# Optimization experiments

Measured on AMD Instinct MI355X. Metric: run time of the kernel, lower is better.

The kernel has to match this reference:

```python
import jax, jax.numpy as jnp
import numpy as np

NEMB = 128
N_NODES = 8192
N_EDGES = 16384
N_STEMS = 4096
N_GRAPHS = 256
N_BLOCKS = 105       # BlockDictionary.n_unique_blocks
N_STEMTYPES = 32     # BlockDictionary.n_stem_types
OUT_PER_STEM = 105
OUT_PER_STOP = 1
NUM_CONV_STEPS = 12
SLOPE = 0.01         # nn.LeakyReLU default negative slope


def _act(v):
    return jax.nn.leaky_relu(v, SLOPE)


def setup_inputs() -> dict:
    key = jax.random.key(0)
    ks = jax.random.split(key, 32)
    def p(i, shape, fan_in):
        return jax.random.normal(ks[i], shape, jnp.float32) / np.sqrt(fan_in).astype(np.float32)
    D = NEMB
    inp = {
        "x": jax.random.randint(ks[0], (N_NODES,), 0, N_BLOCKS + 1),
        "stemtypes": jax.random.randint(ks[1], (N_STEMS,), 0, N_STEMTYPES + 1),
        "edge_attr": jax.random.randint(ks[2], (N_EDGES, 2), 0, N_STEMTYPES),
        "edge_index": jax.random.randint(ks[3], (2, N_EDGES), 0, N_NODES),
        "stem_node_idx": jax.random.randint(ks[4], (N_STEMS,), 0, N_NODES),
        "node_batch": jnp.sort(jax.random.randint(ks[5], (N_NODES,), 0, N_GRAPHS)),
        # embedding tables
        "emb_block": p(6, (N_BLOCKS + 1, D), D),
        "emb_stem": p(7, (N_STEMTYPES + 1, D), D),
        "emb_bond": p(8, (N_STEMTYPES, D), D),
        # block2emb MLP
        "b2e_w1": p(9, (D, D), D), "b2e_b1": p(10, (D,), D),
        "b2e_w2": p(11, (D, D), D), "b2e_b2": p(12, (D,), D),
        # NNConv root weight + bias (edge-nn is identity: nn.Sequential())
        "conv_root": p(13, (D, D), D), "conv_bias": p(14, (D,), D),
        # GRU (torch gate order r, z, n)
        "gru_w_ih": p(15, (3 * D, D), D), "gru_w_hh": p(16, (3 * D, D), D),
        "gru_b_ih": p(17, (3 * D,), D), "gru_b_hh": p(18, (3 * D,), D),
        # stem2pred MLP (in = 2*D)
        "s2p_w1": p(19, (D, 2 * D), 2 * D), "s2p_b1": p(20, (D,), 2 * D),
        "s2p_w2": p(21, (D, D), D), "s2p_b2": p(22, (D,), D),
        "s2p_w3": p(23, (OUT_PER_STEM, D), D), "s2p_b3": p(24, (OUT_PER_STEM,), D),
        # global2pred MLP
        "g2p_w1": p(25, (D, D), D), "g2p_b1": p(26, (D,), D),
        "g2p_w2": p(27, (OUT_PER_STOP, D), D), "g2p_b2": p(28, (OUT_PER_STOP,), D),
    }
    return inp


def reference(x, stemtypes, edge_attr, edge_index, stem_node_idx, node_batch,
              emb_block, emb_stem, emb_bond,
              b2e_w1, b2e_b1, b2e_w2, b2e_b2,
              conv_root, conv_bias,
              gru_w_ih, gru_w_hh, gru_b_ih, gru_b_hh,
              s2p_w1, s2p_b1, s2p_w2, s2p_b2, s2p_w3, s2p_b3,
              g2p_w1, g2p_b1, g2p_w2, g2p_b2):
    block_emb = emb_block[x]                          # [N, D]
    stem_emb = emb_stem[stemtypes]                    # [S, D]
    be = emb_bond[edge_attr]                          # [E, 2, D]
    # outer product -> per-edge [D_in, D_out] weight (matches view(-1, in, out))
    W_e = be[:, 0, :, None] * be[:, 1, None, :]       # [E, D, D]

    out = _act(block_emb @ b2e_w1.T + b2e_b1) @ b2e_w2.T + b2e_b2  # [N, D]
    h = out                                           # GRU hidden state

    src, dst = edge_index[0], edge_index[1]
    ones_e = jnp.ones((N_EDGES,), out.dtype)
    deg = jax.ops.segment_sum(ones_e, dst, num_segments=N_NODES)
    inv_deg = jnp.where(deg > 0, 1.0 / jnp.maximum(deg, 1.0), 0.0)[:, None]

    for _ in range(NUM_CONV_STEPS):
        # NNConv: mean_j (x_j @ W_e) + x @ root + bias, then LeakyReLU
        msg = jnp.einsum('ei,eij->ej', out[src], W_e)                  # [E, D]
        agg = jax.ops.segment_sum(msg, dst, num_segments=N_NODES) * inv_deg
        m = _act(agg + out @ conv_root + conv_bias)
        # single-layer GRU, seq_len = 1
        gi = m @ gru_w_ih.T + gru_b_ih
        gh = h @ gru_w_hh.T + gru_b_hh
        ir, iz, inn = jnp.split(gi, 3, axis=-1)
        hr, hz, hn = jnp.split(gh, 3, axis=-1)
        r = jax.nn.sigmoid(ir + hr)
        z = jax.nn.sigmoid(iz + hz)
        n = jnp.tanh(inn + r * hn)
        h = (1.0 - z) * n + z * h
        out = h

    stem_cat = jnp.concatenate([out[stem_node_idx], stem_emb], axis=1)  # [S, 2D]
    s = _act(stem_cat @ s2p_w1.T + s2p_b1)
    s = _act(s @ s2p_w2.T + s2p_b2)
    stem_pred = s @ s2p_w3.T + s2p_b3                                   # [S, out_per_stem]

    # global_mean_pool
    gsum = jax.ops.segment_sum(out, node_batch, num_segments=N_GRAPHS)
    gcnt = jax.ops.segment_sum(jnp.ones((N_NODES,), out.dtype), node_batch, num_segments=N_GRAPHS)
    gmean = gsum / jnp.maximum(gcnt, 1.0)[:, None]
    g = _act(gmean @ g2p_w1.T + g2p_b1)
    stop_pred = g @ g2p_w2.T + g2p_b2                                   # [G, out_per_stop]
    return stem_pred, stop_pred
```

## Files before the change

kernel.cpp:

```cpp
#include <hip/hip_runtime.h>
#include <math.h>

#define D 128
#define NNODES 8192
#define NEDGES 16384
#define NSTEMS 4096
#define NGRAPHS 256
#define NSTEPS 12
#define OPS 105
#define SLOPE 0.01f
#define MT 32
#define NB (NNODES / MT)
#define ECAP 512
#define LDA 136
#define LDA2 264
#define LDQ 40
#define LDH 132

typedef _Float16 half_t;
typedef __attribute__((ext_vector_type(8))) _Float16 f16x8;
typedef __attribute__((ext_vector_type(4))) float f32x4;

__device__ __forceinline__ float leaky(float x) { return x > 0.f ? x : SLOPE * x; }
__device__ __forceinline__ float fast_sigmoid(float x) {
    return __builtin_amdgcn_rcpf(1.f + __expf(-x));
}
__device__ __forceinline__ float fast_tanh(float x) {
    float e = __expf(2.f * x);
    return 1.f - 2.f * __builtin_amdgcn_rcpf(e + 1.f);
}

__device__ __forceinline__ void gbar_arrive(int* bar, int sync_no) {
    __syncthreads();
    if (threadIdx.x == 0) {
        int grp = blockIdx.x >> 5;
        int old = __hip_atomic_fetch_add(&bar[grp * 32], 1,
                                         __ATOMIC_RELEASE, __HIP_MEMORY_SCOPE_AGENT);
        if (old == sync_no * 32 - 1) {
            int r = __hip_atomic_fetch_add(&bar[256], 1,
                                           __ATOMIC_RELEASE, __HIP_MEMORY_SCOPE_AGENT);
            if (r == sync_no * 8 - 1)
                __hip_atomic_store(&bar[288], sync_no,
                                   __ATOMIC_RELEASE, __HIP_MEMORY_SCOPE_AGENT);
        }
    }
}
__device__ __forceinline__ void gbar_wait(int* bar, int sync_no) {
    if (threadIdx.x == 0) {
        while (__hip_atomic_load(&bar[288], __ATOMIC_RELAXED,
                                 __HIP_MEMORY_SCOPE_AGENT) < sync_no)
            __builtin_amdgcn_s_sleep(1);
    }
    __syncthreads();
}

__global__ void k_setup(
    const float* __restrict__ root, const float* __restrict__ wih,
    const float* __restrict__ whh, const float* __restrict__ bond,
    const float* __restrict__ sw1, const float* __restrict__ sw2,
    const float* __restrict__ sw3, const float* __restrict__ bw1,
    const float* __restrict__ bw2, const float* __restrict__ gw1,
    half_t* __restrict__ rootP, half_t* __restrict__ WihP,
    half_t* __restrict__ WhhP, half_t* __restrict__ bondTP,
    half_t* __restrict__ s1P, half_t* __restrict__ s2P, half_t* __restrict__ s3P,
    half_t* __restrict__ w1P, half_t* __restrict__ w2P, half_t* __restrict__ bondQP,
    float* __restrict__ g1T, int* __restrict__ zeroi) {
    int idx = blockIdx.x * 256 + threadIdx.x;
    int which = blockIdx.y;
    if (which == 10) {
        if (idx < 128 * 128) {
            int r = idx >> 7, c = idx & 127;
            g1T[c * 128 + r] = gw1[idx];
        }
        return;
    }
    if (which == 11) {
        if (idx < 512) zeroi[idx] = 0;
        return;
    }
    int KT = (which == 4) ? 8 : (which == 9) ? 1 : 4;
    int NT = (which == 1 || which == 2) ? 24 : (which == 3) ? 2 : (which == 6) ? 7 : 8;
    if (idx >= NT * KT * 512) return;
    int j = idx & 7;
    int L = (idx >> 3) & 63;
    int t = idx >> 9;
    int kt = t % KT, nt = t / KT;
    int k = kt * 32 + (L >> 4) * 8 + j;
    int n = nt * 16 + (L & 15);
    switch (which) {
        case 0: rootP[idx] = (half_t)root[k * D + n]; break;
        case 1: WihP[idx] = (half_t)wih[n * D + k]; break;
        case 2: WhhP[idx] = (half_t)whh[n * D + k]; break;
        case 3: bondTP[idx] = (half_t)bond[n * D + k]; break;
        case 4: s1P[idx] = (half_t)sw1[n * 256 + k]; break;
        case 5: s2P[idx] = (half_t)sw2[n * 128 + k]; break;
        case 6: s3P[idx] = (n < OPS) ? (half_t)sw3[n * 128 + k] : (half_t)0.f; break;
        case 7: w1P[idx] = (half_t)bw1[n * D + k]; break;
        case 8: w2P[idx] = (half_t)bw2[n * D + k]; break;
        case 9: bondQP[idx] = (half_t)bond[k * D + n]; break;
    }
}

__device__ __forceinline__ int lower_bound_dev(const int* a, int n, int v) {
    int lo = 0, hi = n;
    while (lo < hi) {
        int m = (lo + hi) >> 1;
        if (a[m] < v) lo = m + 1;
        else hi = m;
    }
    return lo;
}

__global__ __launch_bounds__(512, 2) void k_fused(
    const int* __restrict__ x, const float* __restrict__ embBlock,
    const half_t* __restrict__ w1P, const float* __restrict__ b1i,
    const half_t* __restrict__ w2P, const float* __restrict__ b2i,
    const half_t* __restrict__ rootP, const half_t* __restrict__ WihP,
    const half_t* __restrict__ WhhP, const half_t* __restrict__ bondTP,
    const half_t* __restrict__ bondQP,
    const float* __restrict__ cbias, const float* __restrict__ bih,
    const float* __restrict__ bhh,
    const int* __restrict__ eidx, const int* __restrict__ eattr,
    float* __restrict__ Pbuf0, float* __restrict__ Pbuf1,
    float* __restrict__ hF,
    const int* __restrict__ sni, const int* __restrict__ stypes,
    const float* __restrict__ embStem,
    const half_t* __restrict__ s1P, const float* __restrict__ sb1,
    const half_t* __restrict__ s2P, const float* __restrict__ sb2,
    const half_t* __restrict__ s3P, const float* __restrict__ sb3,
    const int* __restrict__ batch, const float* __restrict__ g1T,
    const float* __restrict__ gb1, const float* __restrict__ gw2,
    const float* __restrict__ gb2, float* __restrict__ dout,
    int* __restrict__ bar) {
    __shared__ __align__(16) half_t As[MT * LDA];
    __shared__ __align__(16) half_t Am[MT * LDA];
    __shared__ __align__(16) float Hs[MT * LDH];
    __shared__ __align__(16) half_t Qh[MT * LDQ];
    __shared__ __align__(16) float Q[MT * 32];
    __shared__ __align__(16) int4 elist[ECAP];
    __shared__ int degs_s[MT];
    __shared__ int ecnt;

    const int tid = threadIdx.x;
    const int w = tid >> 6;
    const int lane = tid & 63;
    const int quad = lane >> 4;
    const int l16 = lane & 15;
    const int n0 = blockIdx.x * MT;
    const int c = w * 16 + l16;

    if (tid < MT) degs_s[tid] = 0;
    if (tid == 0) ecnt = 0;
    Q[tid] = 0.f;
    Q[tid + 512] = 0.f;
    __syncthreads();

    {
        int row = tid >> 4;
        int col = (tid & 15) * 8;
        const float* src = embBlock + (size_t)x[n0 + row] * D + col;
        float4 v0 = ((const float4*)src)[0];
        float4 v1 = ((const float4*)src)[1];
        f16x8 hv;
        hv[0] = (half_t)v0.x; hv[1] = (half_t)v0.y; hv[2] = (half_t)v0.z; hv[3] = (half_t)v0.w;
        hv[4] = (half_t)v1.x; hv[5] = (half_t)v1.y; hv[6] = (half_t)v1.z; hv[7] = (half_t)v1.w;
        *(f16x8*)&As[row * LDA + col] = hv;
    }
    for (int e = tid; e < NEDGES; e += 512) {
        int dd = eidx[NEDGES + e];
        unsigned r = (unsigned)(dd - n0);
        if (r < MT) {
            int slot = atomicAdd(&ecnt, 1);
            atomicAdd(&degs_s[r], 1);
            if (slot < ECAP) {
                int2 aa = *(const int2*)(eattr + 2 * e);
                elist[slot] = make_int4(eidx[e], aa.x, aa.y, (int)r);
            }
        }
    }
    f16x8 rootB[4], ghB[12], aggB, bondTB[4];
#pragma unroll
    for (int kt = 0; kt < 4; ++kt)
        rootB[kt] = *(const f16x8*)(rootP + (size_t)((w * 4 + kt) * 64 + lane) * 8);
#pragma unroll
    for (int kt = 0; kt < 4; ++kt)
#pragma unroll
        for (int g = 0; g < 3; ++g)
            ghB[g * 4 + kt] = *(const f16x8*)(WhhP + (size_t)(((g * 8 + w) * 4 + kt) * 64 + lane) * 8);
    aggB = *(const f16x8*)(bondQP + (size_t)(w * 64 + lane) * 8);
    {
        const int ntb = w & 1;
#pragma unroll
        for (int kt = 0; kt < 4; ++kt)
            bondTB[kt] = *(const f16x8*)(bondTP + (size_t)((ntb * 4 + kt) * 64 + lane) * 8);
    }
    const float cb = cbias[c];
    const float bi0 = bih[c], bi1 = bih[D + c], bi2 = bih[2 * D + c];
    const float bh0 = bhh[c], bh1 = bhh[D + c], bh2 = bhh[2 * D + c];
    __syncthreads();

    int4 ep = make_int4(0, 0, 0, 0);
    float idg = 0.f;
    const int m = min(ecnt, ECAP);
    const bool have = (tid < m);
    if (have) {
        ep = elist[tid];
        idg = 1.0f / (float)degs_s[ep.w];
    }

    {
        f32x4 acc[2] = {{0.f, 0.f, 0.f, 0.f}, {0.f, 0.f, 0.f, 0.f}};
#pragma unroll
        for (int kt = 0; kt < 4; ++kt) {
            f16x8 b = *(const f16x8*)(w1P + (size_t)((w * 4 + kt) * 64 + lane) * 8);
            f16x8 a0 = *(const f16x8*)&As[(0 + l16) * LDA + kt * 32 + quad * 8];
            f16x8 a1 = *(const f16x8*)&As[(16 + l16) * LDA + kt * 32 + quad * 8];
            acc[0] = __builtin_amdgcn_mfma_f32_16x16x32_f16(a0, b, acc[0], 0, 0, 0);
            acc[1] = __builtin_amdgcn_mfma_f32_16x16x32_f16(a1, b, acc[1], 0, 0, 0);
        }
        float bb = b1i[c];
#pragma unroll
        for (int mt = 0; mt < 2; ++mt)
#pragma unroll
            for (int r = 0; r < 4; ++r)
                Am[(mt * 16 + quad * 4 + r) * LDA + c] = (half_t)leaky(acc[mt][r] + bb);
    }
    __syncthreads();
    {
        f32x4 acc[2] = {{0.f, 0.f, 0.f, 0.f}, {0.f, 0.f, 0.f, 0.f}};
#pragma unroll
        for (int kt = 0; kt < 4; ++kt) {
            f16x8 b = *(const f16x8*)(w2P + (size_t)((w * 4 + kt) * 64 + lane) * 8);
            f16x8 a0 = *(const f16x8*)&Am[(0 + l16) * LDA + kt * 32 + quad * 8];
            f16x8 a1 = *(const f16x8*)&Am[(16 + l16) * LDA + kt * 32 + quad * 8];
            acc[0] = __builtin_amdgcn_mfma_f32_16x16x32_f16(a0, b, acc[0], 0, 0, 0);
            acc[1] = __builtin_amdgcn_mfma_f32_16x16x32_f16(a1, b, acc[1], 0, 0, 0);
        }
        float bb = b2i[c];
#pragma unroll
        for (int mt = 0; mt < 2; ++mt)
#pragma unroll
            for (int r = 0; r < 4; ++r) {
                int row = mt * 16 + quad * 4 + r;
                float h = acc[mt][r] + bb;
                Hs[row * LDH + c] = h;
                As[row * LDA + c] = (half_t)h;
            }
    }
    __syncthreads();
    if (w < 4) {
        int mt = w >> 1;
        f32x4 acc = {0.f, 0.f, 0.f, 0.f};
#pragma unroll
        for (int kt = 0; kt < 4; ++kt) {
            f16x8 a = *(const f16x8*)&As[(mt * 16 + l16) * LDA + kt * 32 + quad * 8];
            acc = __builtin_amdgcn_mfma_f32_16x16x32_f16(a, bondTB[kt], acc, 0, 0, 0);
        }
#pragma unroll
        for (int r = 0; r < 4; ++r)
            __hip_atomic_store(
                &Pbuf0[(size_t)(n0 + mt * 16 + quad * 4 + r) * 32 + (w & 1) * 16 + l16],
                acc[r], __ATOMIC_RELAXED, __HIP_MEMORY_SCOPE_AGENT);
    }
    gbar_arrive(bar, 1);

    float* Pp = Pbuf0;
    float* Pn = Pbuf1;
    for (int step = 0; step < NSTEPS; ++step) {
        f32x4 ghA[2][3];
#pragma unroll
        for (int mt = 0; mt < 2; ++mt)
#pragma unroll
            for (int g = 0; g < 3; ++g) ghA[mt][g] = f32x4{0.f, 0.f, 0.f, 0.f};
#pragma unroll
        for (int kt = 0; kt < 4; ++kt) {
            f16x8 a0 = *(const f16x8*)&As[(0 + l16) * LDA + kt * 32 + quad * 8];
            f16x8 a1 = *(const f16x8*)&As[(16 + l16) * LDA + kt * 32 + quad * 8];
#pragma unroll
            for (int g = 0; g < 3; ++g) {
                ghA[0][g] = __builtin_amdgcn_mfma_f32_16x16x32_f16(a0, ghB[g * 4 + kt], ghA[0][g], 0, 0, 0);
                ghA[1][g] = __builtin_amdgcn_mfma_f32_16x16x32_f16(a1, ghB[g * 4 + kt], ghA[1][g], 0, 0, 0);
            }
        }
        gbar_wait(bar, step + 1);
        float wv = 0.f;
        if (have)
            wv = __hip_atomic_load(&Pp[(size_t)ep.x * 32 + ep.y],
                                   __ATOMIC_RELAXED, __HIP_MEMORY_SCOPE_AGENT) * idg;
        f32x4 convAcc[2] = {{0.f, 0.f, 0.f, 0.f}, {0.f, 0.f, 0.f, 0.f}};
#pragma unroll
        for (int kt = 0; kt < 4; ++kt) {
            f16x8 a0 = *(const f16x8*)&As[(0 + l16) * LDA + kt * 32 + quad * 8];
            f16x8 a1 = *(const f16x8*)&As[(16 + l16) * LDA + kt * 32 + quad * 8];
            convAcc[0] = __builtin_amdgcn_mfma_f32_16x16x32_f16(a0, rootB[kt], convAcc[0], 0, 0, 0);
            convAcc[1] = __builtin_amdgcn_mfma_f32_16x16x32_f16(a1, rootB[kt], convAcc[1], 0, 0, 0);
        }
        if (have) atomicAdd(&Q[ep.w * 32 + ep.z], wv);
        __syncthreads();

        f16x8 giB[12];
#pragma unroll
        for (int kt = 0; kt < 4; ++kt)
#pragma unroll
            for (int g = 0; g < 3; ++g)
                giB[g * 4 + kt] = *(const f16x8*)(WihP + (size_t)(((g * 8 + w) * 4 + kt) * 64 + lane) * 8);

        Qh[(tid >> 5) * LDQ + (tid & 31)] = (half_t)Q[tid];
        Qh[((tid + 512) >> 5) * LDQ + (tid & 31)] = (half_t)Q[tid + 512];
        __syncthreads();
        Q[tid] = 0.f;
        Q[tid + 512] = 0.f;

#pragma unroll
        for (int mt = 0; mt < 2; ++mt) {
            f32x4 acc = {0.f, 0.f, 0.f, 0.f};
            f16x8 a = *(const f16x8*)&Qh[(mt * 16 + l16) * LDQ + quad * 8];
            acc = __builtin_amdgcn_mfma_f32_16x16x32_f16(a, aggB, acc, 0, 0, 0);
#pragma unroll
            for (int r = 0; r < 4; ++r) {
                float mm = convAcc[mt][r] + cb + acc[r];
                Am[(mt * 16 + quad * 4 + r) * LDA + c] = (half_t)leaky(mm);
            }
        }
        __syncthreads();

        f32x4 giA[2][3];
#pragma unroll
        for (int mt = 0; mt < 2; ++mt)
#pragma unroll
            for (int g = 0; g < 3; ++g) giA[mt][g] = f32x4{0.f, 0.f, 0.f, 0.f};
#pragma unroll
        for (int kt = 0; kt < 4; ++kt) {
            f16x8 a0 = *(const f16x8*)&Am[(0 + l16) * LDA + kt * 32 + quad * 8];
            f16x8 a1 = *(const f16x8*)&Am[(16 + l16) * LDA + kt * 32 + quad * 8];
#pragma unroll
            for (int g = 0; g < 3; ++g) {
                giA[0][g] = __builtin_amdgcn_mfma_f32_16x16x32_f16(a0, giB[g * 4 + kt], giA[0][g], 0, 0, 0);
                giA[1][g] = __builtin_amdgcn_mfma_f32_16x16x32_f16(a1, giB[g * 4 + kt], giA[1][g], 0, 0, 0);
            }
        }
#pragma unroll
        for (int mt = 0; mt < 2; ++mt) {
#pragma unroll
            for (int r = 0; r < 4; ++r) {
                int row = mt * 16 + quad * 4 + r;
                float rg = fast_sigmoid(giA[mt][0][r] + bi0 + ghA[mt][0][r] + bh0);
                float z = fast_sigmoid(giA[mt][1][r] + bi1 + ghA[mt][1][r] + bh1);
                float nn = fast_tanh(giA[mt][2][r] + bi2 + rg * (ghA[mt][2][r] + bh2));
                float hnew = (1.f - z) * nn + z * Hs[row * LDH + c];
                Hs[row * LDH + c] = hnew;
                As[row * LDA + c] = (half_t)hnew;
            }
        }
        __syncthreads();

        if (step < NSTEPS - 1) {
            if (w < 4) {
                int mt = w >> 1;
                f32x4 acc = {0.f, 0.f, 0.f, 0.f};
#pragma unroll
                for (int kt = 0; kt < 4; ++kt) {
                    f16x8 a = *(const f16x8*)&As[(mt * 16 + l16) * LDA + kt * 32 + quad * 8];
                    acc = __builtin_amdgcn_mfma_f32_16x16x32_f16(a, bondTB[kt], acc, 0, 0, 0);
                }
#pragma unroll
                for (int r = 0; r < 4; ++r)
                    __hip_atomic_store(
                        &Pn[(size_t)(n0 + mt * 16 + quad * 4 + r) * 32 + (w & 1) * 16 + l16],
                        acc[r], __ATOMIC_RELAXED, __HIP_MEMORY_SCOPE_AGENT);
            }
            gbar_arrive(bar, step + 2);
            float* tsw = Pp; Pp = Pn; Pn = tsw;
        }
    }

    half_t* cat = As;
    half_t* t1 = Am;
    half_t* t2 = Am + 16 * LDA;
    const int s0 = blockIdx.x * 16;
    {
        int row = tid >> 4;
        int col = (tid & 15) * 8;
        const unsigned long long* s8 = (const unsigned long long*)&Hs[row * LDH + col];
        unsigned long long* d8 = (unsigned long long*)(hF + (size_t)(n0 + row) * D + col);
#pragma unroll
        for (int q2 = 0; q2 < 4; ++q2)
            __hip_atomic_store(d8 + q2, s8[q2], __ATOMIC_RELAXED, __HIP_MEMORY_SCOPE_AGENT);
    }
    if (tid < 256) {
        int row = tid >> 4;
        int col = (tid & 15) * 8;
        const float* src = embStem + (size_t)stypes[s0 + row] * D + col;
        float4 v0 = ((const float4*)src)[0];
        float4 v1 = ((const float4*)src)[1];
        f16x8 hv;
        hv[0] = (half_t)v0.x; hv[1] = (half_t)v0.y; hv[2] = (half_t)v0.z; hv[3] = (half_t)v0.w;
        hv[4] = (half_t)v1.x; hv[5] = (half_t)v1.y; hv[6] = (half_t)v1.z; hv[7] = (half_t)v1.w;
        *(f16x8*)&cat[row * LDA2 + 128 + col] = hv;
    }
    gbar_arrive(bar, NSTEPS + 1);

    f32x4 accS = {0.f, 0.f, 0.f, 0.f};
#pragma unroll
    for (int kt = 4; kt < 8; ++kt) {
        f16x8 b = *(const f16x8*)(s1P + (size_t)((w * 8 + kt) * 64 + lane) * 8);
        f16x8 a = *(const f16x8*)&cat[l16 * LDA2 + kt * 32 + quad * 8];
        accS = __builtin_amdgcn_mfma_f32_16x16x32_f16(a, b, accS, 0, 0, 0);
    }
    gbar_wait(bar, NSTEPS + 1);

    if (tid < 256) {
        int row = tid >> 4;
        int col = (tid & 15) * 8;
        const float* src = hF + (size_t)sni[s0 + row] * D + col;
        float4 v0 = ((const float4*)src)[0];
        float4 v1 = ((const float4*)src)[1];
        f16x8 hv;
        hv[0] = (half_t)v0.x; hv[1] = (half_t)v0.y; hv[2] = (half_t)v0.z; hv[3] = (half_t)v0.w;
        hv[4] = (half_t)v1.x; hv[5] = (half_t)v1.y; hv[6] = (half_t)v1.z; hv[7] = (half_t)v1.w;
        *(f16x8*)&cat[row * LDA2 + col] = hv;
    }
    __syncthreads();
    {
#pragma unroll
        for (int kt = 0; kt < 4; ++kt) {
            f16x8 b = *(const f16x8*)(s1P + (size_t)((w * 8 + kt) * 64 + lane) * 8);
            f16x8 a = *(const f16x8*)&cat[l16 * LDA2 + kt * 32 + quad * 8];
            accS = __builtin_amdgcn_mfma_f32_16x16x32_f16(a, b, accS, 0, 0, 0);
        }
        float bb = sb1[c];
#pragma unroll
        for (int r = 0; r < 4; ++r)
            t1[(quad * 4 + r) * LDA + c] = (half_t)leaky(accS[r] + bb);
    }
    __syncthreads();
    {
        f32x4 acc = {0.f, 0.f, 0.f, 0.f};
#pragma unroll
        for (int kt = 0; kt < 4; ++kt) {
            f16x8 b = *(const f16x8*)(s2P + (size_t)((w * 4 + kt) * 64 + lane) * 8);
            f16x8 a = *(const f16x8*)&t1[l16 * LDA + kt * 32 + quad * 8];
            acc = __builtin_amdgcn_mfma_f32_16x16x32_f16(a, b, acc, 0, 0, 0);
        }
        float bb = sb2[c];
#pragma unroll
        for (int r = 0; r < 4; ++r)
            t2[(quad * 4 + r) * LDA + c] = (half_t)leaky(acc[r] + bb);
    }
    __syncthreads();
    if (w < 7) {
        f32x4 acc = {0.f, 0.f, 0.f, 0.f};
#pragma unroll
        for (int kt = 0; kt < 4; ++kt) {
            f16x8 b = *(const f16x8*)(s3P + (size_t)((w * 4 + kt) * 64 + lane) * 8);
            f16x8 a = *(const f16x8*)&t2[l16 * LDA + kt * 32 + quad * 8];
            acc = __builtin_amdgcn_mfma_f32_16x16x32_f16(a, b, acc, 0, 0, 0);
        }
        int j = w * 16 + l16;
        if (j < OPS) {
            float bb = sb3[j];
#pragma unroll
            for (int r = 0; r < 4; ++r)
                dout[(size_t)(s0 + quad * 4 + r) * OPS + j] = acc[r] + bb;
        }
    }

    {
        const int g = blockIdx.x;
        const int j = tid & 127;
        const int grp = tid >> 7;
        float* part = Q;
        float* mean_s = Q + 512;
        float* red = Q + 640;
        int lo = lower_bound_dev(batch, NNODES, g);
        int hi = lower_bound_dev(batch, NNODES, g + 1);
        float sum = 0.f;
        for (int n = lo + grp; n < hi; n += 4) sum += hF[(size_t)n * D + j];
        part[grp * 128 + j] = sum;
        __syncthreads();
        if (grp == 0) {
            float denom = (hi > lo) ? (float)(hi - lo) : 1.0f;
            mean_s[j] = (part[j] + part[128 + j] + part[256 + j] + part[384 + j]) / denom;
        }
        __syncthreads();
        float a = 0.f;
        for (int i = grp * 32; i < grp * 32 + 32; ++i) a += mean_s[i] * g1T[i * D + j];
        part[grp * 128 + j] = a;
        __syncthreads();
        if (grp == 0) {
            float aa = part[j] + part[128 + j] + part[256 + j] + part[384 + j] + gb1[j];
            red[j] = leaky(aa) * gw2[j];
        }
        __syncthreads();
        for (int off = 64; off > 0; off >>= 1) {
            if (tid < off) red[tid] += red[tid + off];
            __syncthreads();
        }
        if (tid == 0) dout[NSTEMS * OPS + g] = red[0] + gb2[0];
    }
}

extern "C" void kernel_launch(void* const* d_in, const int* in_sizes, int n_in,
                              void* d_out, int out_size, void* d_ws, size_t ws_size,
                              hipStream_t stream) {
    const int* x = (const int*)d_in[0];
    const int* stypes = (const int*)d_in[1];
    const int* eattr = (const int*)d_in[2];
    const int* eidx = (const int*)d_in[3];
    const int* sni = (const int*)d_in[4];
    const int* batch = (const int*)d_in[5];
    const float* embBlock = (const float*)d_in[6];
    const float* embStem = (const float*)d_in[7];
    const float* embBond = (const float*)d_in[8];
    const float* b2e_w1 = (const float*)d_in[9];
    const float* b2e_b1 = (const float*)d_in[10];
    const float* b2e_w2 = (const float*)d_in[11];
    const float* b2e_b2 = (const float*)d_in[12];
    const float* conv_root = (const float*)d_in[13];
    const float* conv_bias = (const float*)d_in[14];
    const float* gru_w_ih = (const float*)d_in[15];
    const float* gru_w_hh = (const float*)d_in[16];
    const float* gru_b_ih = (const float*)d_in[17];
    const float* gru_b_hh = (const float*)d_in[18];
    const float* s2p_w1 = (const float*)d_in[19];
    const float* s2p_b1 = (const float*)d_in[20];
    const float* s2p_w2 = (const float*)d_in[21];
    const float* s2p_b2 = (const float*)d_in[22];
    const float* s2p_w3 = (const float*)d_in[23];
    const float* s2p_b3 = (const float*)d_in[24];
    const float* g2p_w1 = (const float*)d_in[25];
    const float* g2p_b1 = (const float*)d_in[26];
    const float* g2p_w2 = (const float*)d_in[27];
    const float* g2p_b2 = (const float*)d_in[28];
    float* out_f = (float*)d_out;

    float* W = (float*)d_ws;
    size_t off = 0;
    auto alloc = [&](size_t words) {
        size_t o = off;
        off += (words + 3) & ~(size_t)3;
        return o;
    };
    float* hF = W + alloc(NNODES * D);
    float* P0 = W + alloc(NNODES * 32);
    float* P1 = W + alloc(NNODES * 32);
    half_t* rootP = (half_t*)(W + alloc(16384 / 2));
    half_t* WihP = (half_t*)(W + alloc(49152 / 2));
    half_t* WhhP = (half_t*)(W + alloc(49152 / 2));
    half_t* bondTP = (half_t*)(W + alloc(4096 / 2));
    half_t* s1P = (half_t*)(W + alloc(32768 / 2));
    half_t* s2P = (half_t*)(W + alloc(16384 / 2));
    half_t* s3P = (half_t*)(W + alloc(14336 / 2));
    half_t* w1P = (half_t*)(W + alloc(16384 / 2));
    half_t* w2P = (half_t*)(W + alloc(16384 / 2));
    half_t* bondQP = (half_t*)(W + alloc(4096 / 2));
    float* g1T = W + alloc(128 * 128);
    int* bar = (int*)(W + alloc(512));

    k_setup<<<dim3(192, 12), 256, 0, stream>>>(
        conv_root, gru_w_ih, gru_w_hh, embBond, s2p_w1, s2p_w2, s2p_w3,
        b2e_w1, b2e_w2, g2p_w1,
        rootP, WihP, WhhP, bondTP, s1P, s2P, s3P, w1P, w2P, bondQP,
        g1T, bar);

    k_fused<<<NB, 512, 0, stream>>>(
        x, embBlock,
        w1P, b2e_b1, w2P, b2e_b2,
        rootP, WihP, WhhP, bondTP, bondQP,
        conv_bias, gru_b_ih, gru_b_hh,
        eidx, eattr,
        P0, P1, hF,
        sni, stypes, embStem,
        s1P, s2p_b1, s2P, s2p_b2, s3P, s2p_b3,
        batch, g1T, g2p_b1, g2p_w2, g2p_b2,
        out_f, bar);
}
```

Baseline: 225.4 us.

## Fold weight packing into fused kernel behind a grid barrier, reshape barrier tree

```diff
diff --git a/kernel.cpp b/kernel.cpp
--- a/kernel.cpp
+++ b/kernel.cpp
@@ -14,7 +14,7 @@
 #define ECAP 512
 #define LDA 136
 #define LDA2 264
-#define LDQ 40
+#define LDQ2 34
 #define LDH 132
 
 typedef _Float16 half_t;
@@ -33,91 +33,99 @@
 __device__ __forceinline__ void gbar_arrive(int* bar, int sync_no) {
     __syncthreads();
     if (threadIdx.x == 0) {
-        int grp = blockIdx.x >> 5;
+        int grp = blockIdx.x >> 4;
         int old = __hip_atomic_fetch_add(&bar[grp * 32], 1,
                                          __ATOMIC_RELEASE, __HIP_MEMORY_SCOPE_AGENT);
-        if (old == sync_no * 32 - 1) {
-            int r = __hip_atomic_fetch_add(&bar[256], 1,
+        if (old == sync_no * 16 - 1) {
+            int r = __hip_atomic_fetch_add(&bar[512], 1,
                                            __ATOMIC_RELEASE, __HIP_MEMORY_SCOPE_AGENT);
-            if (r == sync_no * 8 - 1)
-                __hip_atomic_store(&bar[288], sync_no,
+            if (r == sync_no * 16 - 1)
+                __hip_atomic_store(&bar[544], sync_no,
                                    __ATOMIC_RELEASE, __HIP_MEMORY_SCOPE_AGENT);
         }
     }
 }
 __device__ __forceinline__ void gbar_wait(int* bar, int sync_no) {
     if (threadIdx.x == 0) {
-        while (__hip_atomic_load(&bar[288], __ATOMIC_RELAXED,
+        while (__hip_atomic_load(&bar[544], __ATOMIC_RELAXED,
                                  __HIP_MEMORY_SCOPE_AGENT) < sync_no)
             __builtin_amdgcn_s_sleep(1);
     }
     __syncthreads();
 }
 
-__global__ void k_setup(
+__device__ __forceinline__ int lower_bound_dev(const int* a, int n, int v) {
+    int lo = 0, hi = n;
+    while (lo < hi) {
+        int m = (lo + hi) >> 1;
+        if (a[m] < v) lo = m + 1;
+        else hi = m;
+    }
+    return lo;
+}
+
+__device__ __forceinline__ void pack_pair(
+    int p,
     const float* __restrict__ root, const float* __restrict__ wih,
     const float* __restrict__ whh, const float* __restrict__ bond,
     const float* __restrict__ sw1, const float* __restrict__ sw2,
     const float* __restrict__ sw3, const float* __restrict__ bw1,
-    const float* __restrict__ bw2, const float* __restrict__ gw1,
+    const float* __restrict__ bw2,
     half_t* __restrict__ rootP, half_t* __restrict__ WihP,
     half_t* __restrict__ WhhP, half_t* __restrict__ bondTP,
     half_t* __restrict__ s1P, half_t* __restrict__ s2P, half_t* __restrict__ s3P,
-    half_t* __restrict__ w1P, half_t* __restrict__ w2P, half_t* __restrict__ bondQP,
-    float* __restrict__ g1T, int* __restrict__ zeroi) {
-    int idx = blockIdx.x * 256 + threadIdx.x;
-    int which = blockIdx.y;
-    if (which == 10) {
-        if (idx < 128 * 128) {
-            int r = idx >> 7, c = idx & 127;
-            g1T[c * 128 + r] = gw1[idx];
-        }
-        return;
-    }
-    if (which == 11) {
-        if (idx < 512) zeroi[idx] = 0;
-        return;
-    }
-    int KT = (which == 4) ? 8 : (which == 9) ? 1 : 4;
-    int NT = (which == 1 || which == 2) ? 24 : (which == 3) ? 2 : (which == 6) ? 7 : 8;
-    if (idx >= NT * KT * 512) return;
+    half_t* __restrict__ w1P, half_t* __restrict__ w2P,
+    half_t* __restrict__ bondQP) {
+    const float* src;
+    half_t* dst;
+    int base, KT = 4, srcld = 128;
+    bool strided = false, guard = false;
+    if (p < 8192)        { base = 0;      dst = rootP;  src = root; strided = true; }
+    else if (p < 32768)  { base = 8192;   dst = WihP;   src = wih; }
+    else if (p < 57344)  { base = 32768;  dst = WhhP;   src = whh; }
+    else if (p < 59392)  { base = 57344;  dst = bondTP; src = bond; }
+    else if (p < 75776)  { base = 59392;  dst = s1P;    src = sw1; KT = 8; srcld = 256; }
+    else if (p < 83968)  { base = 75776;  dst = s2P;    src = sw2; }
+    else if (p < 91136)  { base = 83968;  dst = s3P;    src = sw3; guard = true; }
+    else if (p < 99328)  { base = 91136;  dst = w1P;    src = bw1; }
+    else if (p < 107520) { base = 99328;  dst = w2P;    src = bw2; }
+    else                 { base = 107520; dst = bondQP; src = bond; KT = 1; strided = true; }
+    int idx = (p - base) * 2;
     int j = idx & 7;
     int L = (idx >> 3) & 63;
     int t = idx >> 9;
     int kt = t % KT, nt = t / KT;
     int k = kt * 32 + (L >> 4) * 8 + j;
     int n = nt * 16 + (L & 15);
-    switch (which) {
-        case 0: rootP[idx] = (half_t)root[k * D + n]; break;
-        case 1: WihP[idx] = (half_t)wih[n * D + k]; break;
-        case 2: WhhP[idx] = (half_t)whh[n * D + k]; break;
-        case 3: bondTP[idx] = (half_t)bond[n * D + k]; break;
-        case 4: s1P[idx] = (half_t)sw1[n * 256 + k]; break;
-        case 5: s2P[idx] = (half_t)sw2[n * 128 + k]; break;
-        case 6: s3P[idx] = (n < OPS) ? (half_t)sw3[n * 128 + k] : (half_t)0.f; break;
-        case 7: w1P[idx] = (half_t)bw1[n * D + k]; break;
-        case 8: w2P[idx] = (half_t)bw2[n * D + k]; break;
-        case 9: bondQP[idx] = (half_t)bond[k * D + n]; break;
-    }
-}
-
-__device__ __forceinline__ int lower_bound_dev(const int* a, int n, int v) {
-    int lo = 0, hi = n;
-    while (lo < hi) {
-        int m = (lo + hi) >> 1;
-        if (a[m] < v) lo = m + 1;
-        else hi = m;
-    }
-    return lo;
+    float v0, v1;
+    if (strided) {
+        v0 = src[(size_t)k * 128 + n];
+        v1 = src[(size_t)(k + 1) * 128 + n];
+    } else if (guard && n >= OPS) {
+        v0 = 0.f; v1 = 0.f;
+    } else {
+        float2 vv = *(const float2*)(src + (size_t)n * srcld + k);
+        v0 = vv.x; v1 = vv.y;
+    }
+    union { unsigned u; half_t h[2]; } pk;
+    pk.h[0] = (half_t)v0; pk.h[1] = (half_t)v1;
+    __hip_atomic_store((unsigned*)(dst + idx), pk.u,
+                       __ATOMIC_RELAXED, __HIP_MEMORY_SCOPE_AGENT);
 }
 
 __global__ __launch_bounds__(512, 2) void k_fused(
     const int* __restrict__ x, const float* __restrict__ embBlock,
-    const half_t* __restrict__ w1P, const float* __restrict__ b1i,
-    const half_t* __restrict__ w2P, const float* __restrict__ b2i,
-    const half_t* __restrict__ rootP, const half_t* __restrict__ WihP,
-    const half_t* __restrict__ WhhP, const half_t* __restrict__ bondTP,
-    const half_t* __restrict__ bondQP,
+    const float* __restrict__ rootW, const float* __restrict__ wihW,
+    const float* __restrict__ whhW, const float* __restrict__ bondW,
+    const float* __restrict__ sw1W, const float* __restrict__ sw2W,
+    const float* __restrict__ sw3W, const float* __restrict__ bw1W,
+    const float* __restrict__ bw2W, const float* __restrict__ gw1W,
+    half_t* __restrict__ rootP, half_t* __restrict__ WihP,
+    half_t* __restrict__ WhhP, half_t* __restrict__ bondTP,
+    half_t* __restrict__ s1P, half_t* __restrict__ s2P, half_t* __restrict__ s3P,
+    half_t* __restrict__ w1P, half_t* __restrict__ w2P, half_t* __restrict__ bondQP,
+    float* __restrict__ g1T,
+    const float* __restrict__ b1i, const float* __restrict__ b2i,
     const float* __restrict__ cbias, const float* __restrict__ bih,
     const float* __restrict__ bhh,
     const int* __restrict__ eidx, const int* __restrict__ eattr,
@@ -125,18 +133,16 @@
     float* __restrict__ hF,
     const int* __restrict__ sni, const int* __restrict__ stypes,
     const float* __restrict__ embStem,
-    const half_t* __restrict__ s1P, const float* __restrict__ sb1,
-    const half_t* __restrict__ s2P, const float* __restrict__ sb2,
-    const half_t* __restrict__ s3P, const float* __restrict__ sb3,
-    const int* __restrict__ batch, const float* __restrict__ g1T,
+    const float* __restrict__ sb1, const float* __restrict__ sb2,
+    const float* __restrict__ sb3,
+    const int* __restrict__ batch,
     const float* __restrict__ gb1, const float* __restrict__ gw2,
     const float* __restrict__ gb2, float* __restrict__ dout,
     int* __restrict__ bar) {
     __shared__ __align__(16) half_t As[MT * LDA];
     __shared__ __align__(16) half_t Am[MT * LDA];
     __shared__ __align__(16) float Hs[MT * LDH];
-    __shared__ __align__(16) half_t Qh[MT * LDQ];
-    __shared__ __align__(16) float Q[MT * 32];
+    __shared__ __align__(16) float Q[MT * LDQ2];
     __shared__ __align__(16) int4 elist[ECAP];
     __shared__ int degs_s[MT];
     __shared__ int ecnt;
@@ -151,9 +157,21 @@
 
     if (tid < MT) degs_s[tid] = 0;
     if (tid == 0) ecnt = 0;
-    Q[tid] = 0.f;
-    Q[tid + 512] = 0.f;
-    __syncthreads();
+    for (int i = tid; i < MT * LDQ2; i += 512) Q[i] = 0.f;
+
+    {
+        int g = blockIdx.x * 512 + tid;
+        if (g < 109568) {
+            pack_pair(g, rootW, wihW, whhW, bondW, sw1W, sw2W, sw3W, bw1W, bw2W,
+                      rootP, WihP, WhhP, bondTP, s1P, s2P, s3P, w1P, w2P, bondQP);
+        } else if (g < 125952) {
+            int idx = g - 109568;
+            int r = idx >> 7, cc = idx & 127;
+            __hip_atomic_store(&g1T[cc * 128 + r], gw1W[idx],
+                               __ATOMIC_RELAXED, __HIP_MEMORY_SCOPE_AGENT);
+        }
+    }
+    gbar_arrive(bar, 1);
 
     {
         int row = tid >> 4;
@@ -166,18 +184,29 @@
         hv[4] = (half_t)v1.x; hv[5] = (half_t)v1.y; hv[6] = (half_t)v1.z; hv[7] = (half_t)v1.w;
         *(f16x8*)&As[row * LDA + col] = hv;
     }
-    for (int e = tid; e < NEDGES; e += 512) {
-        int dd = eidx[NEDGES + e];
-        unsigned r = (unsigned)(dd - n0);
-        if (r < MT) {
-            int slot = atomicAdd(&ecnt, 1);
-            atomicAdd(&degs_s[r], 1);
-            if (slot < ECAP) {
-                int2 aa = *(const int2*)(eattr + 2 * e);
-                elist[slot] = make_int4(eidx[e], aa.x, aa.y, (int)r);
+    {
+        const int4* dst4 = (const int4*)(eidx + NEDGES);
+        for (int e4 = tid; e4 < NEDGES / 4; e4 += 512) {
+            int4 dd = dst4[e4];
+            int eb = e4 * 4;
+            int dv[4] = {dd.x, dd.y, dd.z, dd.w};
+#pragma unroll
+            for (int q2 = 0; q2 < 4; ++q2) {
+                unsigned r = (unsigned)(dv[q2] - n0);
+                if (r < MT) {
+                    int slot = atomicAdd(&ecnt, 1);
+                    atomicAdd(&degs_s[r], 1);
+                    if (slot < ECAP) {
+                        int e = eb + q2;
+                        int2 aa = *(const int2*)(eattr + 2 * e);
+                        elist[slot] = make_int4(eidx[e], aa.x, aa.y, (int)r);
+                    }
+                }
             }
         }
     }
+    gbar_wait(bar, 1);
+
     f16x8 rootB[4], ghB[12], aggB, bondTB[4];
 #pragma unroll
     for (int kt = 0; kt < 4; ++kt)
@@ -197,7 +226,6 @@
     const float cb = cbias[c];
     const float bi0 = bih[c], bi1 = bih[D + c], bi2 = bih[2 * D + c];
     const float bh0 = bhh[c], bh1 = bhh[D + c], bh2 = bhh[2 * D + c];
-    __syncthreads();
 
     int4 ep = make_int4(0, 0, 0, 0);
     float idg = 0.f;
@@ -262,7 +290,7 @@
                 &Pbuf0[(size_t)(n0 + mt * 16 + quad * 4 + r) * 32 + (w & 1) * 16 + l16],
                 acc[r], __ATOMIC_RELAXED, __HIP_MEMORY_SCOPE_AGENT);
     }
-    gbar_arrive(bar, 1);
+    gbar_arrive(bar, 2);
 
     float* Pp = Pbuf0;
     float* Pn = Pbuf1;
@@ -282,7 +310,7 @@
                 ghA[1][g] = __builtin_amdgcn_mfma_f32_16x16x32_f16(a1, ghB[g * 4 + kt], ghA[1][g], 0, 0, 0);
             }
         }
-        gbar_wait(bar, step + 1);
+        gbar_wait(bar, step + 2);
         float wv = 0.f;
         if (have)
             wv = __hip_atomic_load(&Pp[(size_t)ep.x * 32 + ep.y],
@@ -295,7 +323,7 @@
             convAcc[0] = __builtin_amdgcn_mfma_f32_16x16x32_f16(a0, rootB[kt], convAcc[0], 0, 0, 0);
             convAcc[1] = __builtin_amdgcn_mfma_f32_16x16x32_f16(a1, rootB[kt], convAcc[1], 0, 0, 0);
         }
-        if (have) atomicAdd(&Q[ep.w * 32 + ep.z], wv);
+        if (have) atomicAdd(&Q[ep.w * LDQ2 + ep.z], wv);
         __syncthreads();
 
         f16x8 giB[12];
@@ -304,17 +332,13 @@
 #pragma unroll
             for (int g = 0; g < 3; ++g)
                 giB[g * 4 + kt] = *(const f16x8*)(WihP + (size_t)(((g * 8 + w) * 4 + kt) * 64 + lane) * 8);
-
-        Qh[(tid >> 5) * LDQ + (tid & 31)] = (half_t)Q[tid];
-        Qh[((tid + 512) >> 5) * LDQ + (tid & 31)] = (half_t)Q[tid + 512];
-        __syncthreads();
-        Q[tid] = 0.f;
-        Q[tid + 512] = 0.f;
-
 #pragma unroll
         for (int mt = 0; mt < 2; ++mt) {
+            const float* qrow = &Q[(mt * 16 + l16) * LDQ2 + quad * 8];
+            f16x8 a;
+#pragma unroll
+            for (int jj = 0; jj < 8; ++jj) a[jj] = (half_t)qrow[jj];
             f32x4 acc = {0.f, 0.f, 0.f, 0.f};
-            f16x8 a = *(const f16x8*)&Qh[(mt * 16 + l16) * LDQ + quad * 8];
             acc = __builtin_amdgcn_mfma_f32_16x16x32_f16(a, aggB, acc, 0, 0, 0);
 #pragma unroll
             for (int r = 0; r < 4; ++r) {
@@ -324,6 +348,8 @@
         }
         __syncthreads();
 
+        if (step < NSTEPS - 1)
+            for (int i = tid; i < MT * LDQ2; i += 512) Q[i] = 0.f;
         f32x4 giA[2][3];
 #pragma unroll
         for (int mt = 0; mt < 2; ++mt)
@@ -369,7 +395,7 @@
                         &Pn[(size_t)(n0 + mt * 16 + quad * 4 + r) * 32 + (w & 1) * 16 + l16],
                         acc[r], __ATOMIC_RELAXED, __HIP_MEMORY_SCOPE_AGENT);
             }
-            gbar_arrive(bar, step + 2);
+            gbar_arrive(bar, step + 3);
             float* tsw = Pp; Pp = Pn; Pn = tsw;
         }
     }
@@ -398,7 +424,7 @@
         hv[4] = (half_t)v1.x; hv[5] = (half_t)v1.y; hv[6] = (half_t)v1.z; hv[7] = (half_t)v1.w;
         *(f16x8*)&cat[row * LDA2 + 128 + col] = hv;
     }
-    gbar_arrive(bar, NSTEPS + 1);
+    gbar_arrive(bar, NSTEPS + 2);
 
     f32x4 accS = {0.f, 0.f, 0.f, 0.f};
 #pragma unroll
@@ -407,7 +433,7 @@
         f16x8 a = *(const f16x8*)&cat[l16 * LDA2 + kt * 32 + quad * 8];
         accS = __builtin_amdgcn_mfma_f32_16x16x32_f16(a, b, accS, 0, 0, 0);
     }
-    gbar_wait(bar, NSTEPS + 1);
+    gbar_wait(bar, NSTEPS + 2);
 
     if (tid < 256) {
         int row = tid >> 4;
@@ -555,23 +581,21 @@
     half_t* w2P = (half_t*)(W + alloc(16384 / 2));
     half_t* bondQP = (half_t*)(W + alloc(4096 / 2));
     float* g1T = W + alloc(128 * 128);
-    int* bar = (int*)(W + alloc(512));
-
-    k_setup<<<dim3(192, 12), 256, 0, stream>>>(
-        conv_root, gru_w_ih, gru_w_hh, embBond, s2p_w1, s2p_w2, s2p_w3,
-        b2e_w1, b2e_w2, g2p_w1,
-        rootP, WihP, WhhP, bondTP, s1P, s2P, s3P, w1P, w2P, bondQP,
-        g1T, bar);
+    int* bar = (int*)(W + alloc(1024));
+
+    hipMemsetAsync(bar, 0, 4096, stream);
 
     k_fused<<<NB, 512, 0, stream>>>(
         x, embBlock,
-        w1P, b2e_b1, w2P, b2e_b2,
-        rootP, WihP, WhhP, bondTP, bondQP,
+        conv_root, gru_w_ih, gru_w_hh, embBond,
+        s2p_w1, s2p_w2, s2p_w3, b2e_w1, b2e_w2, g2p_w1,
+        rootP, WihP, WhhP, bondTP, s1P, s2P, s3P, w1P, w2P, bondQP, g1T,
+        b2e_b1, b2e_b2,
         conv_bias, gru_b_ih, gru_b_hh,
         eidx, eattr,
         P0, P1, hF,
         sni, stypes, embStem,
-        s1P, s2p_b1, s2P, s2p_b2, s3P, s2p_b3,
-        batch, g1T, g2p_b1, g2p_w2, g2p_b2,
+        s2p_b1, s2p_b2, s2p_b3,
+        batch, g2p_b1, g2p_w2, g2p_b2,
         out_f, bar);
 }
```

Result: slower. 237.0 us (+5.1%).

## Restructure grid barrier tree, drop Qh staging sync, hoist Wih fragments, vectorize edge scan

Applied to the files above, without the earlier changes.

```diff
diff --git a/kernel.cpp b/kernel.cpp
--- a/kernel.cpp
+++ b/kernel.cpp
@@ -14,7 +14,7 @@
 #define ECAP 512
 #define LDA 136
 #define LDA2 264
-#define LDQ 40
+#define LDQ2 34
 #define LDH 132
 
 typedef _Float16 half_t;
@@ -33,21 +33,21 @@
 __device__ __forceinline__ void gbar_arrive(int* bar, int sync_no) {
     __syncthreads();
     if (threadIdx.x == 0) {
-        int grp = blockIdx.x >> 5;
+        int grp = blockIdx.x >> 4;
         int old = __hip_atomic_fetch_add(&bar[grp * 32], 1,
                                          __ATOMIC_RELEASE, __HIP_MEMORY_SCOPE_AGENT);
-        if (old == sync_no * 32 - 1) {
-            int r = __hip_atomic_fetch_add(&bar[256], 1,
+        if (old == sync_no * 16 - 1) {
+            int r = __hip_atomic_fetch_add(&bar[512], 1,
                                            __ATOMIC_RELEASE, __HIP_MEMORY_SCOPE_AGENT);
-            if (r == sync_no * 8 - 1)
-                __hip_atomic_store(&bar[288], sync_no,
+            if (r == sync_no * 16 - 1)
+                __hip_atomic_store(&bar[544], sync_no,
                                    __ATOMIC_RELEASE, __HIP_MEMORY_SCOPE_AGENT);
         }
     }
 }
 __device__ __forceinline__ void gbar_wait(int* bar, int sync_no) {
     if (threadIdx.x == 0) {
-        while (__hip_atomic_load(&bar[288], __ATOMIC_RELAXED,
+        while (__hip_atomic_load(&bar[544], __ATOMIC_RELAXED,
                                  __HIP_MEMORY_SCOPE_AGENT) < sync_no)
             __builtin_amdgcn_s_sleep(1);
     }
@@ -75,7 +75,7 @@
         return;
     }
     if (which == 11) {
-        if (idx < 512) zeroi[idx] = 0;
+        if (idx < 1024) zeroi[idx] = 0;
         return;
     }
     int KT = (which == 4) ? 8 : (which == 9) ? 1 : 4;
@@ -135,8 +135,7 @@
     __shared__ __align__(16) half_t As[MT * LDA];
     __shared__ __align__(16) half_t Am[MT * LDA];
     __shared__ __align__(16) float Hs[MT * LDH];
-    __shared__ __align__(16) half_t Qh[MT * LDQ];
-    __shared__ __align__(16) float Q[MT * 32];
+    __shared__ __align__(16) float Q[MT * LDQ2];
     __shared__ __align__(16) int4 elist[ECAP];
     __shared__ int degs_s[MT];
     __shared__ int ecnt;
@@ -151,8 +150,7 @@
 
     if (tid < MT) degs_s[tid] = 0;
     if (tid == 0) ecnt = 0;
-    Q[tid] = 0.f;
-    Q[tid + 512] = 0.f;
+    for (int i = tid; i < MT * LDQ2; i += 512) Q[i] = 0.f;
     __syncthreads();
 
     {
@@ -166,19 +164,28 @@
         hv[4] = (half_t)v1.x; hv[5] = (half_t)v1.y; hv[6] = (half_t)v1.z; hv[7] = (half_t)v1.w;
         *(f16x8*)&As[row * LDA + col] = hv;
     }
-    for (int e = tid; e < NEDGES; e += 512) {
-        int dd = eidx[NEDGES + e];
-        unsigned r = (unsigned)(dd - n0);
-        if (r < MT) {
-            int slot = atomicAdd(&ecnt, 1);
-            atomicAdd(&degs_s[r], 1);
-            if (slot < ECAP) {
-                int2 aa = *(const int2*)(eattr + 2 * e);
-                elist[slot] = make_int4(eidx[e], aa.x, aa.y, (int)r);
-            }
-        }
-    }
-    f16x8 rootB[4], ghB[12], aggB, bondTB[4];
+    {
+        const int4* dst4 = (const int4*)(eidx + NEDGES);
+        for (int e4 = tid; e4 < NEDGES / 4; e4 += 512) {
+            int4 dd = dst4[e4];
+            int eb = e4 * 4;
+            int dv[4] = {dd.x, dd.y, dd.z, dd.w};
+#pragma unroll
+            for (int q2 = 0; q2 < 4; ++q2) {
+                unsigned r = (unsigned)(dv[q2] - n0);
+                if (r < MT) {
+                    int slot = atomicAdd(&ecnt, 1);
+                    atomicAdd(&degs_s[r], 1);
+                    if (slot < ECAP) {
+                        int e = eb + q2;
+                        int2 aa = *(const int2*)(eattr + 2 * e);
+                        elist[slot] = make_int4(eidx[e], aa.x, aa.y, (int)r);
+                    }
+                }
+            }
+        }
+    }
+    f16x8 rootB[4], ghB[12], giB[12], aggB, bondTB[4];
 #pragma unroll
     for (int kt = 0; kt < 4; ++kt)
         rootB[kt] = *(const f16x8*)(rootP + (size_t)((w * 4 + kt) * 64 + lane) * 8);
@@ -187,6 +194,11 @@
 #pragma unroll
         for (int g = 0; g < 3; ++g)
             ghB[g * 4 + kt] = *(const f16x8*)(WhhP + (size_t)(((g * 8 + w) * 4 + kt) * 64 + lane) * 8);
+#pragma unroll
+    for (int kt = 0; kt < 4; ++kt)
+#pragma unroll
+        for (int g = 0; g < 3; ++g)
+            giB[g * 4 + kt] = *(const f16x8*)(WihP + (size_t)(((g * 8 + w) * 4 + kt) * 64 + lane) * 8);
     aggB = *(const f16x8*)(bondQP + (size_t)(w * 64 + lane) * 8);
     {
         const int ntb = w & 1;
@@ -295,26 +307,16 @@
             convAcc[0] = __builtin_amdgcn_mfma_f32_16x16x32_f16(a0, rootB[kt], convAcc[0], 0, 0, 0);
             convAcc[1] = __builtin_amdgcn_mfma_f32_16x16x32_f16(a1, rootB[kt], convAcc[1], 0, 0, 0);
         }
-        if (have) atomicAdd(&Q[ep.w * 32 + ep.z], wv);
-        __syncthreads();
-
-        f16x8 giB[12];
-#pragma unroll
-        for (int kt = 0; kt < 4; ++kt)
-#pragma unroll
-            for (int g = 0; g < 3; ++g)
-                giB[g * 4 + kt] = *(const f16x8*)(WihP + (size_t)(((g * 8 + w) * 4 + kt) * 64 + lane) * 8);
-
-        Qh[(tid >> 5) * LDQ + (tid & 31)] = (half_t)Q[tid];
-        Qh[((tid + 512) >> 5) * LDQ + (tid & 31)] = (half_t)Q[tid + 512];
-        __syncthreads();
-        Q[tid] = 0.f;
-        Q[tid + 512] = 0.f;
+        if (have) atomicAdd(&Q[ep.w * LDQ2 + ep.z], wv);
+        __syncthreads();
 
 #pragma unroll
         for (int mt = 0; mt < 2; ++mt) {
+            const float* qrow = &Q[(mt * 16 + l16) * LDQ2 + quad * 8];
+            f16x8 a;
+#pragma unroll
+            for (int jj = 0; jj < 8; ++jj) a[jj] = (half_t)qrow[jj];
             f32x4 acc = {0.f, 0.f, 0.f, 0.f};
-            f16x8 a = *(const f16x8*)&Qh[(mt * 16 + l16) * LDQ + quad * 8];
             acc = __builtin_amdgcn_mfma_f32_16x16x32_f16(a, aggB, acc, 0, 0, 0);
 #pragma unroll
             for (int r = 0; r < 4; ++r) {
@@ -324,6 +326,8 @@
         }
         __syncthreads();
 
+        if (step < NSTEPS - 1)
+            for (int i = tid; i < MT * LDQ2; i += 512) Q[i] = 0.f;
         f32x4 giA[2][3];
 #pragma unroll
         for (int mt = 0; mt < 2; ++mt)
@@ -555,7 +559,7 @@
     half_t* w2P = (half_t*)(W + alloc(16384 / 2));
     half_t* bondQP = (half_t*)(W + alloc(4096 / 2));
     float* g1T = W + alloc(128 * 128);
-    int* bar = (int*)(W + alloc(512));
+    int* bar = (int*)(W + alloc(1024));
 
     k_setup<<<dim3(192, 12), 256, 0, stream>>>(
         conv_root, gru_w_ih, gru_w_hh, embBond, s2p_w1, s2p_w2, s2p_w3,
```

New measurement: 219.8 us (median of 2 runs). -2.5%, faster.
